# Kernel tuning notes

Measured on AMD Instinct MI355X. Metric: run time of the kernel, lower is better.

Reference implementation:

```python
import jax, jax.numpy as jnp
import numpy as np

N = 100_000   # nodes
E = 1_600_000 # edges (avg degree 16)
D = 32        # input = hidden = output channels (module defaults)
L = 3         # num_layers


def setup_inputs() -> dict:
    key = jax.random.key(0)
    ks = jax.random.split(key, 6)
    X = jax.random.normal(ks[0], (N, D), jnp.float32)
    edge_index = jax.random.randint(ks[1], (2, E), 0, N)
    edge_weight = jax.random.uniform(ks[2], (E,), jnp.float32)
    # 8 GCNConv layers per GConvLSTM: x_i, h_i, x_f, h_f, x_c, h_c, x_o, h_o
    conv_w = jax.random.normal(ks[3], (L, 8, D, D), jnp.float32) * np.float32(1.0 / np.sqrt(D))
    conv_b = jnp.zeros((L, 8, D), jnp.float32)
    # peephole weights w_c_i, w_c_f, w_c_o (glorot) and biases b_i, b_f, b_c, b_o (zeros)
    wc = jax.random.normal(ks[4], (L, 3, D), jnp.float32) * np.float32(0.1)
    bg = jnp.zeros((L, 4, D), jnp.float32)
    return dict(X=X, edge_index=edge_index, edge_weight=edge_weight,
                conv_w=conv_w, conv_b=conv_b, wc=wc, bg=bg)


def _gcn_norm(edge_index, edge_weight, n):
    # PyG gcn_norm (sym): add self loops with weight 1, then D^-1/2 A D^-1/2
    loop = jnp.arange(n)
    src = jnp.concatenate([edge_index[0], loop])
    dst = jnp.concatenate([edge_index[1], loop])
    w = jnp.concatenate([edge_weight, jnp.ones((n,), edge_weight.dtype)])
    deg = jax.ops.segment_sum(w, dst, num_segments=n)
    dinv = jnp.where(deg > 0, jax.lax.rsqrt(deg), jnp.zeros_like(deg))
    return src, dst, dinv[src] * w * dinv[dst]


def reference(X, edge_index, edge_weight, conv_w, conv_b, wc, bg):
    n = X.shape[0]
    src, dst, nw = _gcn_norm(edge_index, edge_weight, n)

    def gcn(x, W, b):
        xw = x @ W                                   # [N, D] linear transform
        agg = jax.ops.segment_sum(nw[:, None] * xw[src], dst, num_segments=n)
        return agg + b

    out = X
    for l in range(conv_w.shape[0]):
        x = out
        H = jnp.zeros((n, conv_w.shape[-1]), x.dtype)  # hidden state init (None -> zeros)
        C = jnp.zeros_like(H)                          # cell state init
        Wl, bl = conv_w[l], conv_b[l]
        I = jax.nn.sigmoid(gcn(x, Wl[0], bl[0]) + gcn(H, Wl[1], bl[1]) + wc[l, 0] * C + bg[l, 0])
        F = jax.nn.sigmoid(gcn(x, Wl[2], bl[2]) + gcn(H, Wl[3], bl[3]) + wc[l, 1] * C + bg[l, 1])
        T = jnp.tanh(gcn(x, Wl[4], bl[4]) + gcn(H, Wl[5], bl[5]) + bg[l, 2])
        C = F * C + I * T
        O = jax.nn.sigmoid(gcn(x, Wl[6], bl[6]) + gcn(H, Wl[7], bl[7]) + wc[l, 2] * C + bg[l, 3])
        out = O * jnp.tanh(C)
    return out
```

## Files before the change

### kernel.cpp

```cpp
#include <hip/hip_runtime.h>
#include <math.h>

#define TPB 256
#define NBMAX 2048

__device__ __forceinline__ float fsig(float x) {
    return __builtin_amdgcn_rcpf(1.f + __expf(-x));
}
__device__ __forceinline__ float ftanh(float x) {
    float t = __expf(2.f * fabsf(x));
    float r = 1.f - 2.f * __builtin_amdgcn_rcpf(t + 1.f);
    return copysignf(r, x);
}

__global__ __launch_bounds__(256) void k_zero(int* __restrict__ p, int n) {
    int i = blockIdx.x * 256 + threadIdx.x;
    if (i < n) p[i] = 0;
}


__global__ __launch_bounds__(256) void k_bhist(const int* __restrict__ ei,
                                               int* __restrict__ bhist, int E, int NB) {
    __shared__ int h[NBMAX];
    for (int i = threadIdx.x; i < NB; i += 256) h[i] = 0;
    __syncthreads();
    int stride = gridDim.x * 256;
    for (int e = blockIdx.x * 256 + threadIdx.x; e < E; e += stride)
        atomicAdd(&h[ei[E + e] >> 8], 1);
    __syncthreads();
    for (int i = threadIdx.x; i < NB; i += 256) if (h[i]) atomicAdd(&bhist[i], h[i]);
}

__global__ __launch_bounds__(256) void k_bscan(const int* __restrict__ bhist,
                                               int* __restrict__ bbase, int* __restrict__ bfill,
                                               int NB, int E) {
    __shared__ int tsum[256];
    int tid = threadIdx.x;
    int per = (NB + 255) / 256;
    int loc[8]; int tot = 0;
    int base = tid * per;
#pragma unroll
    for (int j = 0; j < 8; j++) {
        int i = base + j;
        int v = (j < per && i < NB) ? bhist[i] : 0;
        loc[j] = v; tot += v;
    }
    tsum[tid] = tot;
    __syncthreads();
    for (int off = 1; off < 256; off <<= 1) {
        int t = (tid >= off) ? tsum[tid - off] : 0;
        __syncthreads();
        tsum[tid] += t;
        __syncthreads();
    }
    int run = tsum[tid] - tot;
#pragma unroll
    for (int j = 0; j < 8; j++) {
        int i = base + j;
        if (j < per && i < NB) { bbase[i] = run; bfill[i] = run; run += loc[j]; }
    }
    if (tid == 0) bbase[NB] = E;
}

__global__ __launch_bounds__(256) void k_bin(const int* __restrict__ ei,
                                             const float* __restrict__ ew,
                                             int* bfill, int2* __restrict__ ebuf,
                                             int E, int NB) {
    __shared__ int h[NBMAX];
    __shared__ int gb[NBMAX];
    const int EPT = 16;
    int tid = threadIdx.x;
    int base = blockIdx.x * 256 * EPT;
    for (int i = tid; i < NB; i += 256) h[i] = 0;
    __syncthreads();
    int src[EPT]; float w[EPT]; int bkt[EPT]; int lrank[EPT];
#pragma unroll
    for (int j = 0; j < EPT; j++) {
        int e = base + j * 256 + tid;
        if (e < E) {
            src[j] = ei[e]; int d = ei[E + e]; w[j] = ew[e];
            int b = d >> 8;
            bkt[j] = b | ((d & 255) << 16);
            lrank[j] = atomicAdd(&h[b], 1);
        } else bkt[j] = -1;
    }
    __syncthreads();
    for (int i = tid; i < NB; i += 256) gb[i] = h[i] ? atomicAdd(&bfill[i], h[i]) : 0;
    __syncthreads();
#pragma unroll
    for (int j = 0; j < EPT; j++) {
        if (bkt[j] >= 0) {
            int b = bkt[j] & 0xFFFF, dlow = (bkt[j] >> 16) & 0xFF;
            int2 v; v.x = src[j] | (dlow << 24); v.y = __float_as_int(w[j]);
            ebuf[gb[b] + lrank[j]] = v;
        }
    }
}

__global__ __launch_bounds__(256) void k_bucket(const int2* __restrict__ ebuf,
                                                const int* __restrict__ bbase,
                                                int2* __restrict__ esl,
                                                int4* __restrict__ ovbuf,
                                                int* __restrict__ ovcnt,
                                                float* __restrict__ dinv,
                                                const float4* __restrict__ X4,
                                                float4* __restrict__ Y4,
                                                int N, int E) {
    __shared__ int lcnt[256];
    __shared__ float wsum[256];
    __shared__ float sdinv[256];
    int b = blockIdx.x, tid = threadIdx.x;
    int beg = bbase[b], end = bbase[b + 1];
    lcnt[tid] = 0; wsum[tid] = 0.f;
    __syncthreads();
    size_t nodeBase = (size_t)(b << 8) * 32;
    for (int i = beg + tid; i < end; i += 256) {
        int2 v = ebuf[i];
        int dlow = ((unsigned)v.x) >> 24;
        unsafeAtomicAdd(&wsum[dlow], __int_as_float(v.y));
        int rank = atomicAdd(&lcnt[dlow], 1);
        int2 o; o.x = v.x & 0x00FFFFFF; o.y = v.y;
        if (rank < 32) {
            esl[nodeBase + dlow * 32 + rank] = o;
        } else {
            int oi = atomicAdd(ovcnt, 1);
            int4 q; q.x = o.x; q.y = (b << 8) + dlow; q.z = o.y; q.w = 0;
            ovbuf[oi] = q;
        }
    }
    __syncthreads();
    float dv = rsqrtf(1.0f + wsum[tid]);
    sdinv[tid] = dv;
    int node = (b << 8) + tid;
    if (node < N) dinv[node] = dv;
    int nNodes = N - (b << 8); if (nNodes > 256) nNodes = 256;
    for (int i = tid; i < nNodes * 32; i += 256) {
        int r = i >> 5, j = i & 31;
        if (j >= lcnt[r]) { int2 z; z.x = 0; z.y = 0; esl[nodeBase + i] = z; }
    }
    int limit = nNodes * 8;
    size_t base4 = ((size_t)b << 8) * 8;
    for (int i = tid; i < limit; i += 256) {
        float4 v = X4[base4 + i];
        float d = sdinv[i >> 3];
        float4 o; o.x = v.x * d; o.y = v.y * d; o.z = v.z * d; o.w = v.w * d;
        Y4[base4 + i] = o;
    }
}


__global__ __launch_bounds__(256) void k_gather(const float4* __restrict__ Y4,
                                                const int2* __restrict__ esl,
                                                const float* __restrict__ dinv,
                                                float4* __restrict__ AX4, int N) {
    int wid = (blockIdx.x * blockDim.x + threadIdx.x) >> 6;
    if (wid >= N) return;
    int lane = threadIdx.x & 63;
    int q = lane >> 3, c4 = lane & 7;
    const int2* ep = esl + (size_t)wid * 32 + q;
    int2 p0 = ep[0], p1 = ep[8], p2 = ep[16], p3 = ep[24];
    float di = dinv[wid];
    float4 self = Y4[(size_t)wid * 8 + c4];
    float4 y0 = Y4[(size_t)p0.x * 8 + c4];
    float4 y1 = Y4[(size_t)p1.x * 8 + c4];
    float4 y2 = Y4[(size_t)p2.x * 8 + c4];
    float4 y3 = Y4[(size_t)p3.x * 8 + c4];
    float w0 = __int_as_float(p0.y), w1 = __int_as_float(p1.y);
    float w2 = __int_as_float(p2.y), w3 = __int_as_float(p3.y);
    float4 acc1, acc2;
    if (q == 0) acc1 = self; else { acc1.x = acc1.y = acc1.z = acc1.w = 0.f; }
    acc2.x = acc2.y = acc2.z = acc2.w = 0.f;
    acc1.x += w0 * y0.x; acc1.y += w0 * y0.y; acc1.z += w0 * y0.z; acc1.w += w0 * y0.w;
    acc2.x += w1 * y1.x; acc2.y += w1 * y1.y; acc2.z += w1 * y1.z; acc2.w += w1 * y1.w;
    acc1.x += w2 * y2.x; acc1.y += w2 * y2.y; acc1.z += w2 * y2.z; acc1.w += w2 * y2.w;
    acc2.x += w3 * y3.x; acc2.y += w3 * y3.y; acc2.z += w3 * y3.z; acc2.w += w3 * y3.w;
    acc1.x += acc2.x; acc1.y += acc2.y; acc1.z += acc2.z; acc1.w += acc2.w;
#pragma unroll
    for (int off = 8; off <= 32; off <<= 1) {
        acc1.x += __shfl_xor(acc1.x, off);
        acc1.y += __shfl_xor(acc1.y, off);
        acc1.z += __shfl_xor(acc1.z, off);
        acc1.w += __shfl_xor(acc1.w, off);
    }
    if (lane < 8) {
        float4 o; o.x = acc1.x * di; o.y = acc1.y * di; o.z = acc1.z * di; o.w = acc1.w * di;
        AX4[(size_t)wid * 8 + c4] = o;
    }
}

__global__ __launch_bounds__(256) void k_tail(const float* __restrict__ Y,
                                              const int4* __restrict__ ovbuf,
                                              const int* __restrict__ ovcnt,
                                              const float* __restrict__ dinv,
                                              float* __restrict__ AX) {
    int cnt = *ovcnt;
    int total = cnt * 32;
    int stride = gridDim.x * 256;
    for (int i = blockIdx.x * 256 + threadIdx.x; i < total; i += stride) {
        int e = i >> 5, c = i & 31;
        int4 q = ovbuf[e];
        int src = q.x, dst = q.y;
        float w = __int_as_float(q.z);
        atomicAdd(&AX[(size_t)dst * 32 + c], dinv[dst] * w * Y[(size_t)src * 32 + c]);
    }
}

__global__ __launch_bounds__(256) void k_gates(const float* __restrict__ AX,
                                               const float* __restrict__ cw,
                                               const float* __restrict__ cb,
                                               const float* __restrict__ wc,
                                               const float* __restrict__ bg,
                                               const float* __restrict__ dinv,
                                               float* __restrict__ outRaw,
                                               float* __restrict__ outY,
                                               int N, int l, int isLast) {
    __shared__ float Ws[32][96];
    __shared__ float Xs[128][33];
    __shared__ float bS[96];
    __shared__ float wcs[32];
    __shared__ float sdv[128];
    int tid = threadIdx.x;
    for (int i = tid; i < 3072; i += 256) {
        int k = i / 96, ccol = i - k * 96;
        int g = ccol >> 5, o = ccol & 31;
        int j = (g == 0) ? 0 : ((g == 1) ? 4 : 6);
        Ws[k][ccol] = cw[(((l * 8 + j) * 32) + k) * 32 + o];
    }
    if (tid < 32) {
        int c = tid;
        bS[c]      = cb[((l * 8 + 0) * 32) + c] + cb[((l * 8 + 1) * 32) + c] + bg[((l * 4 + 0) * 32) + c];
        bS[32 + c] = cb[((l * 8 + 4) * 32) + c] + cb[((l * 8 + 5) * 32) + c] + bg[((l * 4 + 2) * 32) + c];
        bS[64 + c] = cb[((l * 8 + 6) * 32) + c] + cb[((l * 8 + 7) * 32) + c] + bg[((l * 4 + 3) * 32) + c];
        wcs[c]     = wc[((l * 3 + 2) * 32) + c];
    }
    int row0 = blockIdx.x * 128;
    for (int i = tid; i < 4096; i += 256) {
        int r = i >> 5, k = i & 31; int gr = row0 + r;
        Xs[r][k] = (gr < N) ? AX[(size_t)gr * 32 + k] : 0.f;
    }
    if (tid < 128) {
        int gr = row0 + tid;
        sdv[tid] = (gr < N) ? dinv[gr] : 0.f;
    }
    __syncthreads();
    int r0 = tid >> 3, g8 = tid & 7, cbase = g8 * 4;
    float aI[4][4], aT[4][4], aO[4][4];
#pragma unroll
    for (int j = 0; j < 4; j++)
#pragma unroll
        for (int cc = 0; cc < 4; cc++) { aI[j][cc] = 0.f; aT[j][cc] = 0.f; aO[j][cc] = 0.f; }
#pragma unroll 4
    for (int k = 0; k < 32; k++) {
        float4 wI = *(const float4*)&Ws[k][cbase];
        float4 wT = *(const float4*)&Ws[k][32 + cbase];
        float4 wO = *(const float4*)&Ws[k][64 + cbase];
#pragma unroll
        for (int j = 0; j < 4; j++) {
            float xv = Xs[r0 + 32 * j][k];
            aI[j][0] += xv * wI.x; aI[j][1] += xv * wI.y; aI[j][2] += xv * wI.z; aI[j][3] += xv * wI.w;
            aT[j][0] += xv * wT.x; aT[j][1] += xv * wT.y; aT[j][2] += xv * wT.z; aT[j][3] += xv * wT.w;
            aO[j][0] += xv * wO.x; aO[j][1] += xv * wO.y; aO[j][2] += xv * wO.z; aO[j][3] += xv * wO.w;
        }
    }
#pragma unroll
    for (int j = 0; j < 4; j++) {
        int r = r0 + 32 * j;
        int gn = row0 + r;
        if (gn >= N) continue;
        float di = sdv[r];
        float4 v;
        float res[4];
#pragma unroll
        for (int cc = 0; cc < 4; cc++) {
            int c = cbase + cc;
            float I = fsig(aI[j][cc] + bS[c]);
            float T = ftanh(aT[j][cc] + bS[32 + c]);
            float C = I * T;
            float O = fsig(aO[j][cc] + wcs[c] * C + bS[64 + c]);
            float val = O * ftanh(C);
            res[cc] = isLast ? val : di * val;
        }
        v.x = res[0]; v.y = res[1]; v.z = res[2]; v.w = res[3];
        float* dst = isLast ? outRaw : outY;
        *(float4*)&dst[(size_t)gn * 32 + cbase] = v;
    }
}

extern "C" void kernel_launch(void* const* d_in, const int* in_sizes, int n_in,
                              void* d_out, int out_size, void* d_ws, size_t ws_size,
                              hipStream_t stream) {
    const float* X  = (const float*)d_in[0];
    const int*   ei = (const int*)d_in[1];
    const float* ew = (const float*)d_in[2];
    const float* cw = (const float*)d_in[3];
    const float* cb = (const float*)d_in[4];
    const float* wc = (const float*)d_in[5];
    const float* bg = (const float*)d_in[6];
    int N = in_sizes[0] / 32;
    int E = in_sizes[2];
    int L = in_sizes[3] / (8 * 32 * 32);
    float* out = (float*)d_out;
    int NB = (N + 255) >> 8;

    char* p = (char*)d_ws;
    auto alloc = [&](size_t bytes) -> char* {
        char* r = p; p += (bytes + 255) & ~(size_t)255; return r;
    };
    int*   bhist     = (int*)alloc((size_t)(NB + 1) * 4);
    int*   bbase     = (int*)alloc((size_t)(NB + 1) * 4);
    int*   bfill     = (int*)alloc((size_t)NB * 4);
    float* dinv      = (float*)alloc((size_t)N * 4);
    int2*  ebuf      = (int2*)alloc((size_t)E * 8);
    int2*  esl       = (int2*)alloc((size_t)N * 32 * 8);
    int4*  ovbuf     = (int4*)alloc((size_t)65536 * 16);
    float* Y         = (float*)alloc((size_t)N * 32 * 4);
    float* AX        = (float*)alloc((size_t)N * 32 * 4);
    int*   ovcnt     = bhist + NB;

    k_zero<<<(NB + 256) / 256, 256, 0, stream>>>(bhist, NB + 1);
    k_bhist<<<512, 256, 0, stream>>>(ei, bhist, E, NB);
    k_bscan<<<1, 256, 0, stream>>>(bhist, bbase, bfill, NB, E);
    int nBin = (E + 4095) / 4096;
    k_bin<<<nBin, 256, 0, stream>>>(ei, ew, bfill, ebuf, E, NB);
    k_bucket<<<NB, 256, 0, stream>>>(ebuf, bbase, esl, ovbuf, ovcnt, dinv,
                                     (const float4*)X, (float4*)Y, N, E);

    for (int l = 0; l < L; l++) {
        k_gather<<<(N + 3) / 4, 256, 0, stream>>>((const float4*)Y, esl, dinv,
                                                  (float4*)AX, N);
        k_tail<<<16, 256, 0, stream>>>(Y, ovbuf, ovcnt, dinv, AX);
        k_gates<<<(N + 127) / 128, 256, 0, stream>>>(AX, cw, cb, wc, bg, dinv,
                                                     out, Y, N, l, l == L - 1);
    }
}
```

Before: 248.0 us.

## Stage per-node edge slots in LDS with 128-node buckets and nontemporal streams

The bucket kernel now builds the padded per-node edge slot list in shared memory and writes it to global memory as coalesced int4 stores. Previously it scattered individual int2 writes and then ran a separate zero-fill pass. To fit the 32 KB slot tile, buckets shrink from 256 to 128 nodes, which doubles the bucket count. Nontemporal loads and stores are added on the streaming edge arrays and slot reads to reduce cache pollution. The change trades more bucket blocks and more LDS per block for fewer uncoalesced global writes.

```diff
diff --git a/kernel.cpp b/kernel.cpp
--- a/kernel.cpp
+++ b/kernel.cpp
@@ -12,6 +12,15 @@
     float r = 1.f - 2.f * __builtin_amdgcn_rcpf(t + 1.f);
     return copysignf(r, x);
 }
+__device__ __forceinline__ int2 nt_load_int2(const int2* p) {
+    long long v = __builtin_nontemporal_load((const long long*)p);
+    int2 r; r.x = (int)(unsigned)(v & 0xFFFFFFFFLL); r.y = (int)(unsigned)((unsigned long long)v >> 32);
+    return r;
+}
+__device__ __forceinline__ void nt_store_int2(int2* p, int2 v) {
+    long long q = ((long long)(unsigned long long)(unsigned)v.y << 32) | (unsigned)v.x;
+    __builtin_nontemporal_store(q, (long long*)p);
+}
 
 __global__ __launch_bounds__(256) void k_zero(int* __restrict__ p, int n) {
     int i = blockIdx.x * 256 + threadIdx.x;
@@ -26,7 +35,7 @@
     __syncthreads();
     int stride = gridDim.x * 256;
     for (int e = blockIdx.x * 256 + threadIdx.x; e < E; e += stride)
-        atomicAdd(&h[ei[E + e] >> 8], 1);
+        atomicAdd(&h[__builtin_nontemporal_load(&ei[E + e]) >> 7], 1);
     __syncthreads();
     for (int i = threadIdx.x; i < NB; i += 256) if (h[i]) atomicAdd(&bhist[i], h[i]);
 }
@@ -78,9 +87,11 @@
     for (int j = 0; j < EPT; j++) {
         int e = base + j * 256 + tid;
         if (e < E) {
-            src[j] = ei[e]; int d = ei[E + e]; w[j] = ew[e];
-            int b = d >> 8;
-            bkt[j] = b | ((d & 255) << 16);
+            src[j] = __builtin_nontemporal_load(&ei[e]);
+            int d = __builtin_nontemporal_load(&ei[E + e]);
+            w[j] = __builtin_nontemporal_load(&ew[e]);
+            int b = d >> 7;
+            bkt[j] = b | ((d & 127) << 16);
             lrank[j] = atomicAdd(&h[b], 1);
         } else bkt[j] = -1;
     }
@@ -90,9 +101,9 @@
 #pragma unroll
     for (int j = 0; j < EPT; j++) {
         if (bkt[j] >= 0) {
-            int b = bkt[j] & 0xFFFF, dlow = (bkt[j] >> 16) & 0xFF;
+            int b = bkt[j] & 0xFFFF, dlow = (bkt[j] >> 16) & 0x7F;
             int2 v; v.x = src[j] | (dlow << 24); v.y = __float_as_int(w[j]);
-            ebuf[gb[b] + lrank[j]] = v;
+            nt_store_int2(&ebuf[gb[b] + lrank[j]], v);
         }
     }
 }
@@ -106,40 +117,45 @@
                                                 const float4* __restrict__ X4,
                                                 float4* __restrict__ Y4,
                                                 int N, int E) {
-    __shared__ int lcnt[256];
-    __shared__ float wsum[256];
-    __shared__ float sdinv[256];
+    __shared__ int2 sl[128 * 32];
+    __shared__ int lcnt[128];
+    __shared__ float wsum[128];
+    __shared__ float sdinv[128];
     int b = blockIdx.x, tid = threadIdx.x;
     int beg = bbase[b], end = bbase[b + 1];
-    lcnt[tid] = 0; wsum[tid] = 0.f;
-    __syncthreads();
-    size_t nodeBase = (size_t)(b << 8) * 32;
+    if (tid < 128) { lcnt[tid] = 0; wsum[tid] = 0.f; }
+    for (int i = tid; i < 4096; i += 256) { int2 z; z.x = 0; z.y = 0; sl[i] = z; }
+    __syncthreads();
     for (int i = beg + tid; i < end; i += 256) {
-        int2 v = ebuf[i];
+        int2 v = nt_load_int2(&ebuf[i]);
         int dlow = ((unsigned)v.x) >> 24;
         unsafeAtomicAdd(&wsum[dlow], __int_as_float(v.y));
         int rank = atomicAdd(&lcnt[dlow], 1);
         int2 o; o.x = v.x & 0x00FFFFFF; o.y = v.y;
         if (rank < 32) {
-            esl[nodeBase + dlow * 32 + rank] = o;
+            sl[dlow * 32 + rank] = o;
         } else {
             int oi = atomicAdd(ovcnt, 1);
-            int4 q; q.x = o.x; q.y = (b << 8) + dlow; q.z = o.y; q.w = 0;
+            int4 q; q.x = o.x; q.y = (b << 7) + dlow; q.z = o.y; q.w = 0;
             ovbuf[oi] = q;
         }
     }
     __syncthreads();
-    float dv = rsqrtf(1.0f + wsum[tid]);
-    sdinv[tid] = dv;
-    int node = (b << 8) + tid;
-    if (node < N) dinv[node] = dv;
-    int nNodes = N - (b << 8); if (nNodes > 256) nNodes = 256;
-    for (int i = tid; i < nNodes * 32; i += 256) {
-        int r = i >> 5, j = i & 31;
-        if (j >= lcnt[r]) { int2 z; z.x = 0; z.y = 0; esl[nodeBase + i] = z; }
-    }
+    int node = (b << 7) + tid;
+    if (tid < 128) {
+        float dv = rsqrtf(1.0f + wsum[tid]);
+        sdinv[tid] = dv;
+        if (node < N) dinv[node] = dv;
+    }
+    __syncthreads();
+    size_t nodeBase4 = (size_t)(b << 7) * 16;
+    const int4* slv = (const int4*)sl;
+    int4* dst4 = (int4*)esl;
+    for (int i = tid; i < 2048; i += 256)
+        dst4[nodeBase4 + i] = slv[i];
+    int nNodes = N - (b << 7); if (nNodes > 128) nNodes = 128;
     int limit = nNodes * 8;
-    size_t base4 = ((size_t)b << 8) * 8;
+    size_t base4 = ((size_t)b << 7) * 8;
     for (int i = tid; i < limit; i += 256) {
         float4 v = X4[base4 + i];
         float d = sdinv[i >> 3];
@@ -158,7 +174,10 @@
     int lane = threadIdx.x & 63;
     int q = lane >> 3, c4 = lane & 7;
     const int2* ep = esl + (size_t)wid * 32 + q;
-    int2 p0 = ep[0], p1 = ep[8], p2 = ep[16], p3 = ep[24];
+    int2 p0 = nt_load_int2(ep);
+    int2 p1 = nt_load_int2(ep + 8);
+    int2 p2 = nt_load_int2(ep + 16);
+    int2 p3 = nt_load_int2(ep + 24);
     float di = dinv[wid];
     float4 self = Y4[(size_t)wid * 8 + c4];
     float4 y0 = Y4[(size_t)p0.x * 8 + c4];
@@ -300,7 +319,7 @@
     int E = in_sizes[2];
     int L = in_sizes[3] / (8 * 32 * 32);
     float* out = (float*)d_out;
-    int NB = (N + 255) >> 8;
+    int NB = (N + 127) >> 7;
 
     char* p = (char*)d_ws;
     auto alloc = [&](size_t bytes) -> char* {
@@ -311,7 +330,7 @@
     int*   bfill     = (int*)alloc((size_t)NB * 4);
     float* dinv      = (float*)alloc((size_t)N * 4);
     int2*  ebuf      = (int2*)alloc((size_t)E * 8);
-    int2*  esl       = (int2*)alloc((size_t)N * 32 * 8);
+    int2*  esl       = (int2*)alloc((size_t)NB * 128 * 32 * 8);
     int4*  ovbuf     = (int4*)alloc((size_t)65536 * 16);
     float* Y         = (float*)alloc((size_t)N * 32 * 4);
     float* AX        = (float*)alloc((size_t)N * 32 * 4);
```

Result: slower. 294.7 us (+18.8%).

## Fuse neighbor gather, overflow tail and gate GEMM into one per-layer kernel

Applied to the files above, without the earlier changes.

Replaces the separate gather, tail-atomic and gates kernels with one kernel per layer. Each wave aggregates 32 nodes' neighbors straight into shared memory, prefetching the next node's edge list, and wave 0 scans the overflow edge list for rows in its block. Y is double-buffered across layers. This removes the AX round trip through global memory and two launches per layer, at the cost of less memory-level parallelism in the gather loop, a per-block serial scan of the overflow list, and only 782 blocks.

```diff
diff --git a/kernel.cpp b/kernel.cpp
--- a/kernel.cpp
+++ b/kernel.cpp
@@ -148,78 +148,25 @@
     }
 }
 
-
-__global__ __launch_bounds__(256) void k_gather(const float4* __restrict__ Y4,
-                                                const int2* __restrict__ esl,
-                                                const float* __restrict__ dinv,
-                                                float4* __restrict__ AX4, int N) {
-    int wid = (blockIdx.x * blockDim.x + threadIdx.x) >> 6;
-    if (wid >= N) return;
-    int lane = threadIdx.x & 63;
-    int q = lane >> 3, c4 = lane & 7;
-    const int2* ep = esl + (size_t)wid * 32 + q;
-    int2 p0 = ep[0], p1 = ep[8], p2 = ep[16], p3 = ep[24];
-    float di = dinv[wid];
-    float4 self = Y4[(size_t)wid * 8 + c4];
-    float4 y0 = Y4[(size_t)p0.x * 8 + c4];
-    float4 y1 = Y4[(size_t)p1.x * 8 + c4];
-    float4 y2 = Y4[(size_t)p2.x * 8 + c4];
-    float4 y3 = Y4[(size_t)p3.x * 8 + c4];
-    float w0 = __int_as_float(p0.y), w1 = __int_as_float(p1.y);
-    float w2 = __int_as_float(p2.y), w3 = __int_as_float(p3.y);
-    float4 acc1, acc2;
-    if (q == 0) acc1 = self; else { acc1.x = acc1.y = acc1.z = acc1.w = 0.f; }
-    acc2.x = acc2.y = acc2.z = acc2.w = 0.f;
-    acc1.x += w0 * y0.x; acc1.y += w0 * y0.y; acc1.z += w0 * y0.z; acc1.w += w0 * y0.w;
-    acc2.x += w1 * y1.x; acc2.y += w1 * y1.y; acc2.z += w1 * y1.z; acc2.w += w1 * y1.w;
-    acc1.x += w2 * y2.x; acc1.y += w2 * y2.y; acc1.z += w2 * y2.z; acc1.w += w2 * y2.w;
-    acc2.x += w3 * y3.x; acc2.y += w3 * y3.y; acc2.z += w3 * y3.z; acc2.w += w3 * y3.w;
-    acc1.x += acc2.x; acc1.y += acc2.y; acc1.z += acc2.z; acc1.w += acc2.w;
-#pragma unroll
-    for (int off = 8; off <= 32; off <<= 1) {
-        acc1.x += __shfl_xor(acc1.x, off);
-        acc1.y += __shfl_xor(acc1.y, off);
-        acc1.z += __shfl_xor(acc1.z, off);
-        acc1.w += __shfl_xor(acc1.w, off);
-    }
-    if (lane < 8) {
-        float4 o; o.x = acc1.x * di; o.y = acc1.y * di; o.z = acc1.z * di; o.w = acc1.w * di;
-        AX4[(size_t)wid * 8 + c4] = o;
-    }
-}
-
-__global__ __launch_bounds__(256) void k_tail(const float* __restrict__ Y,
-                                              const int4* __restrict__ ovbuf,
-                                              const int* __restrict__ ovcnt,
-                                              const float* __restrict__ dinv,
-                                              float* __restrict__ AX) {
-    int cnt = *ovcnt;
-    int total = cnt * 32;
-    int stride = gridDim.x * 256;
-    for (int i = blockIdx.x * 256 + threadIdx.x; i < total; i += stride) {
-        int e = i >> 5, c = i & 31;
-        int4 q = ovbuf[e];
-        int src = q.x, dst = q.y;
-        float w = __int_as_float(q.z);
-        atomicAdd(&AX[(size_t)dst * 32 + c], dinv[dst] * w * Y[(size_t)src * 32 + c]);
-    }
-}
-
-__global__ __launch_bounds__(256) void k_gates(const float* __restrict__ AX,
+__global__ __launch_bounds__(256) void k_layer(const float4* __restrict__ Yin4,
+                                               const int2* __restrict__ esl,
+                                               const float* __restrict__ dinv,
+                                               const int4* __restrict__ ovbuf,
+                                               const int* __restrict__ ovcnt,
                                                const float* __restrict__ cw,
                                                const float* __restrict__ cb,
                                                const float* __restrict__ wc,
                                                const float* __restrict__ bg,
-                                               const float* __restrict__ dinv,
                                                float* __restrict__ outRaw,
                                                float* __restrict__ outY,
                                                int N, int l, int isLast) {
     __shared__ float Ws[32][96];
-    __shared__ float Xs[128][33];
+    __shared__ float Xs[128][36];
     __shared__ float bS[96];
     __shared__ float wcs[32];
     __shared__ float sdv[128];
     int tid = threadIdx.x;
+    int row0 = blockIdx.x * 128;
     for (int i = tid; i < 3072; i += 256) {
         int k = i / 96, ccol = i - k * 96;
         int g = ccol >> 5, o = ccol & 31;
@@ -233,14 +180,77 @@
         bS[64 + c] = cb[((l * 8 + 6) * 32) + c] + cb[((l * 8 + 7) * 32) + c] + bg[((l * 4 + 3) * 32) + c];
         wcs[c]     = wc[((l * 3 + 2) * 32) + c];
     }
-    int row0 = blockIdx.x * 128;
-    for (int i = tid; i < 4096; i += 256) {
-        int r = i >> 5, k = i & 31; int gr = row0 + r;
-        Xs[r][k] = (gr < N) ? AX[(size_t)gr * 32 + k] : 0.f;
-    }
     if (tid < 128) {
         int gr = row0 + tid;
         sdv[tid] = (gr < N) ? dinv[gr] : 0.f;
+    }
+    __syncthreads();
+    int wv = tid >> 6, lane = tid & 63;
+    int q = lane >> 3, c4 = lane & 7;
+    int nbase = wv * 32;
+    int2 p0, p1, p2, p3; float4 self;
+    {
+        int n = row0 + nbase;
+        if (n < N) {
+            const int2* ep = esl + (size_t)n * 32 + q;
+            p0 = ep[0]; p1 = ep[8]; p2 = ep[16]; p3 = ep[24];
+            self = Yin4[(size_t)n * 8 + c4];
+        }
+    }
+    for (int i = 0; i < 32; i++) {
+        int2 a0 = p0, a1 = p1, a2 = p2, a3 = p3;
+        float4 sf = self;
+        int n = row0 + nbase + i;
+        int n1 = n + 1;
+        if (i + 1 < 32 && n1 < N) {
+            const int2* ep = esl + (size_t)n1 * 32 + q;
+            p0 = ep[0]; p1 = ep[8]; p2 = ep[16]; p3 = ep[24];
+            self = Yin4[(size_t)n1 * 8 + c4];
+        }
+        if (n < N) {
+            float4 y0 = Yin4[(size_t)a0.x * 8 + c4];
+            float4 y1 = Yin4[(size_t)a1.x * 8 + c4];
+            float4 y2 = Yin4[(size_t)a2.x * 8 + c4];
+            float4 y3 = Yin4[(size_t)a3.x * 8 + c4];
+            float w0 = __int_as_float(a0.y), w1 = __int_as_float(a1.y);
+            float w2 = __int_as_float(a2.y), w3 = __int_as_float(a3.y);
+            float4 acc1, acc2;
+            if (q == 0) acc1 = sf; else { acc1.x = acc1.y = acc1.z = acc1.w = 0.f; }
+            acc2.x = acc2.y = acc2.z = acc2.w = 0.f;
+            acc1.x += w0 * y0.x; acc1.y += w0 * y0.y; acc1.z += w0 * y0.z; acc1.w += w0 * y0.w;
+            acc2.x += w1 * y1.x; acc2.y += w1 * y1.y; acc2.z += w1 * y1.z; acc2.w += w1 * y1.w;
+            acc1.x += w2 * y2.x; acc1.y += w2 * y2.y; acc1.z += w2 * y2.z; acc1.w += w2 * y2.w;
+            acc2.x += w3 * y3.x; acc2.y += w3 * y3.y; acc2.z += w3 * y3.z; acc2.w += w3 * y3.w;
+            acc1.x += acc2.x; acc1.y += acc2.y; acc1.z += acc2.z; acc1.w += acc2.w;
+#pragma unroll
+            for (int off = 8; off <= 32; off <<= 1) {
+                acc1.x += __shfl_xor(acc1.x, off);
+                acc1.y += __shfl_xor(acc1.y, off);
+                acc1.z += __shfl_xor(acc1.z, off);
+                acc1.w += __shfl_xor(acc1.w, off);
+            }
+            if (lane < 8) {
+                float di = sdv[nbase + i];
+                float4 o; o.x = acc1.x * di; o.y = acc1.y * di;
+                o.z = acc1.z * di; o.w = acc1.w * di;
+                *(float4*)&Xs[nbase + i][c4 * 4] = o;
+            }
+        }
+    }
+    __syncthreads();
+    if (wv == 0) {
+        const float* Yf = (const float*)Yin4;
+        int cnt = *ovcnt;
+        for (int i = 0; i < cnt; i++) {
+            int4 qv = ovbuf[i];
+            int d = qv.y;
+            if (d >= row0 && d < row0 + 128 && d < N) {
+                int nb = d - row0;
+                float w = __int_as_float(qv.z) * sdv[nb];
+                if (lane < 32)
+                    Xs[nb][lane] += w * Yf[(size_t)qv.x * 32 + lane];
+            }
+        }
     }
     __syncthreads();
     int r0 = tid >> 3, g8 = tid & 7, cbase = g8 * 4;
@@ -313,8 +323,8 @@
     int2*  ebuf      = (int2*)alloc((size_t)E * 8);
     int2*  esl       = (int2*)alloc((size_t)N * 32 * 8);
     int4*  ovbuf     = (int4*)alloc((size_t)65536 * 16);
-    float* Y         = (float*)alloc((size_t)N * 32 * 4);
-    float* AX        = (float*)alloc((size_t)N * 32 * 4);
+    float* Ya        = (float*)alloc((size_t)N * 32 * 4);
+    float* Yb        = (float*)alloc((size_t)N * 32 * 4);
     int*   ovcnt     = bhist + NB;
 
     k_zero<<<(NB + 256) / 256, 256, 0, stream>>>(bhist, NB + 1);
@@ -323,13 +333,14 @@
     int nBin = (E + 4095) / 4096;
     k_bin<<<nBin, 256, 0, stream>>>(ei, ew, bfill, ebuf, E, NB);
     k_bucket<<<NB, 256, 0, stream>>>(ebuf, bbase, esl, ovbuf, ovcnt, dinv,
-                                     (const float4*)X, (float4*)Y, N, E);
-
+                                     (const float4*)X, (float4*)Ya, N, E);
+
+    int NBL = (N + 127) / 128;
     for (int l = 0; l < L; l++) {
-        k_gather<<<(N + 3) / 4, 256, 0, stream>>>((const float4*)Y, esl, dinv,
-                                                  (float4*)AX, N);
-        k_tail<<<16, 256, 0, stream>>>(Y, ovbuf, ovcnt, dinv, AX);
-        k_gates<<<(N + 127) / 128, 256, 0, stream>>>(AX, cw, cb, wc, bg, dinv,
-                                                     out, Y, N, l, l == L - 1);
-    }
-}
+        const float* Yin = (l & 1) ? Yb : Ya;
+        float*       Ynx = (l & 1) ? Ya : Yb;
+        k_layer<<<NBL, 256, 0, stream>>>((const float4*)Yin, esl, dinv,
+                                         ovbuf, ovcnt, cw, cb, wc, bg,
+                                         out, Ynx, N, l, l == L - 1);
+    }
+}
```

Measured after the change: 235.0 us. 5.2% less time.
